# Performance work log

Measured on AMD Instinct MI355X. Metric: run time of the kernel, lower is better.

Reference implementation:

```python
import jax, jax.numpy as jnp
import numpy as np

N = 100000        # nodes
E = 1600000       # edges
DIM = 64
HEADS = 8
HEAD_DIM = DIM // HEADS
HIDDEN = 4 * DIM  # hidden_dim_multiplier = 4


def setup_inputs() -> dict:
    key = jax.random.key(0)
    ks = jax.random.split(key, 20)
    s = 0.05
    return {
        "x": jax.random.normal(ks[0], (N, DIM), jnp.float32),
        "edge_feat": jax.random.normal(ks[1], (E, 2), jnp.float32),
        "w_in": jax.random.normal(ks[2], (DIM, DIM), jnp.float32) * s,
        "b_in": jnp.zeros((DIM,), jnp.float32),
        "w_edge": jax.random.normal(ks[3], (2, DIM), jnp.float32) * s,
        "b_edge": jnp.zeros((DIM,), jnp.float32),
        "w_att_u": jax.random.normal(ks[4], (DIM, HEADS), jnp.float32) * s,
        "b_att_u": jnp.zeros((HEADS,), jnp.float32),
        "w_att_v": jax.random.normal(ks[5], (DIM, HEADS), jnp.float32) * s,  # no bias
        "w_att_e": jax.random.normal(ks[6], (DIM, HEADS), jnp.float32) * s,
        "b_att_e": jnp.zeros((HEADS,), jnp.float32),
        "w_ff1": jax.random.normal(ks[7], (DIM, HIDDEN), jnp.float32) * s,
        "b_ff1": jnp.zeros((HIDDEN,), jnp.float32),
        "w_ff2": jax.random.normal(ks[8], (HIDDEN, DIM), jnp.float32) * s,
        "b_ff2": jnp.zeros((DIM,), jnp.float32),
        "src": jax.random.randint(ks[9], (E,), 0, N, jnp.int32),
        "dst": jax.random.randint(ks[10], (E,), 0, N, jnp.int32),
    }


def reference(x, edge_feat, w_in, b_in, w_edge, b_edge, w_att_u, b_att_u,
              w_att_v, w_att_e, b_att_e, w_ff1, b_ff1, w_ff2, b_ff2, src, dst):
    n = x.shape[0]
    h = x @ w_in + b_in                                  # [N, dim]
    ea = edge_feat @ w_edge + b_edge                     # [E, dim]
    su = h @ w_att_u + b_att_u                           # [N, H]
    sv = h @ w_att_v                                     # [N, H] (no bias)
    se = ea @ w_att_e + b_att_e                          # [E, H]
    # u_add_v gather + edge bias + LeakyReLU
    scores = jax.nn.leaky_relu(su[src] + sv[dst] + se, 0.2)  # [E, H]
    # edge softmax over incoming edges of each dst node
    m = jax.ops.segment_max(scores, dst, num_segments=n)     # [N, H]
    m = jnp.where(jnp.isfinite(m), m, 0.0)                   # nodes w/o in-edges
    e = jnp.exp(scores - m[dst])                             # [E, H]
    denom = jax.ops.segment_sum(e, dst, num_segments=n)      # [N, H]
    probs = e / jnp.maximum(denom, 1e-12)[dst]               # [E, H]
    # u_mul_e_sum: weighted scatter-sum of messages
    hv = h.reshape(n, HEAD_DIM, HEADS)                       # [N, hd, H]
    msg = hv[src] * probs[:, None, :]                        # [E, hd, H]
    out = jax.ops.segment_sum(msg, dst, num_segments=n).reshape(n, DIM)
    # feed-forward (dropout=0 at eval)
    out = jax.nn.gelu(out @ w_ff1 + b_ff1, approximate=False) @ w_ff2 + b_ff2
    return out
```

## Files before the change

### kernel.cpp

```cpp
#include <hip/hip_runtime.h>
#include <math.h>

#define DIM 64
#define HEADS 8
#define HIDDEN 256

__device__ __forceinline__ float lane_bcast(float v, int srcLane) {
  return __int_as_float(__builtin_amdgcn_readlane(__float_as_int(v), srcLane));
}

__global__ void prep_kernel(
    const float* __restrict__ w_in, const float* __restrict__ b_in,
    const float* __restrict__ w_edge, const float* __restrict__ b_edge,
    const float* __restrict__ w_att_u, const float* __restrict__ b_att_u,
    const float* __restrict__ w_att_v,
    const float* __restrict__ w_att_e, const float* __restrict__ b_att_e,
    float* __restrict__ Waug, float* __restrict__ baug,
    float* __restrict__ wcc, float* __restrict__ bcc)
{
  int t = threadIdx.x;
  if (t < 64) {
    for (int j = 0; j < 64; ++j) Waug[t*80 + j] = w_in[t*64 + j];
    for (int hh = 0; hh < 8; ++hh) {
      float a = 0.f, b = 0.f;
      for (int j = 0; j < 64; ++j) {
        float w = w_in[t*64 + j];
        a += w * w_att_u[j*8 + hh];
        b += w * w_att_v[j*8 + hh];
      }
      Waug[t*80 + 64 + hh] = a;
      Waug[t*80 + 72 + hh] = b;
    }
  } else if (t < 128) {
    int j = t - 64;
    baug[j] = b_in[j];
  } else if (t < 136) {
    int hh = t - 128;
    float a = b_att_u[hh];
    for (int k = 0; k < 64; ++k) a += b_in[k] * w_att_u[k*8 + hh];
    baug[64 + hh] = a;
  } else if (t < 144) {
    int hh = t - 136;
    float a = 0.f;
    for (int k = 0; k < 64; ++k) a += b_in[k] * w_att_v[k*8 + hh];
    baug[72 + hh] = a;
  } else if (t < 160) {
    int c = (t - 144) >> 3, hh = (t - 144) & 7;
    float a = 0.f;
    for (int j = 0; j < 64; ++j) a += w_edge[c*64 + j] * w_att_e[j*8 + hh];
    wcc[c*8 + hh] = a;
  } else if (t < 168) {
    int hh = t - 160;
    float a = b_att_e[hh];
    for (int j = 0; j < 64; ++j) a += b_edge[j] * w_att_e[j*8 + hh];
    bcc[hh] = a;
  }
}

__global__ __launch_bounds__(256) void node_gemm_kernel(
    const float* __restrict__ x,
    const float* __restrict__ Waug, const float* __restrict__ baug,
    float* __restrict__ hbuf, float* __restrict__ subuf, float* __restrict__ svbuf,
    int n_nodes)
{
  const int wid = threadIdx.x >> 6;
  const int lane = threadIdx.x & 63;
  const long nbase = (long)blockIdx.x * 32 + wid * 8;

  float xr[8];
  #pragma unroll
  for (int m = 0; m < 8; ++m) {
    long n = nbase + m; if (n >= n_nodes) n = n_nodes - 1;
    xr[m] = x[n*DIM + lane];
  }
  const float bmain = baug[lane];
  const float bext  = (lane < 16) ? baug[64 + lane] : 0.f;
  float acc[8], acc2[8];
  #pragma unroll
  for (int m = 0; m < 8; ++m) { acc[m] = bmain; acc2[m] = 0.f; }

  #pragma unroll 16
  for (int k = 0; k < 64; ++k) {
    float wmain = Waug[k*80 + lane];
    float wext  = (lane < 16) ? Waug[k*80 + 64 + lane] : 0.f;
    #pragma unroll
    for (int m = 0; m < 8; ++m) {
      float xk = lane_bcast(xr[m], k);
      acc[m]  += xk * wmain;
      acc2[m] += xk * wext;
    }
  }
  #pragma unroll
  for (int m = 0; m < 8; ++m) {
    long n = nbase + m;
    if (n >= n_nodes) continue;
    hbuf[n*DIM + lane] = acc[m];
    if (lane < 8)       subuf[n*8 + lane]     = acc2[m] + bext;
    else if (lane < 16) svbuf[n*8 + lane - 8] = acc2[m] + bext;
  }
}

__global__ void hist_kernel(const int* __restrict__ dst, int* __restrict__ deg, int n_edges) {
  int i = blockIdx.x * blockDim.x + threadIdx.x;
  if (i < n_edges) atomicAdd(&deg[dst[i]], 1);
}

__global__ void alloc_kernel(const int* __restrict__ deg, int* __restrict__ off,
                             int* __restrict__ counter, int n_nodes) {
  int i = blockIdx.x * blockDim.x + threadIdx.x;
  int lane = threadIdx.x & 63;
  int d = (i < n_nodes) ? deg[i] : 0;
  int pre = d;
  #pragma unroll
  for (int s = 1; s < 64; s <<= 1) {
    int v = __shfl_up(pre, s, 64);
    if (lane >= s) pre += v;
  }
  int tot = __shfl(pre, 63, 64);
  int base = 0;
  if (lane == 0) base = atomicAdd(counter, tot);
  base = __shfl(base, 0, 64);
  if (i < n_nodes) off[i] = base + pre - d;
}

__global__ void scatter_kernel(const int* __restrict__ dst, const int* __restrict__ off,
                               int* __restrict__ pos, int* __restrict__ csr, int n_edges) {
  int i = blockIdx.x * blockDim.x + threadIdx.x;
  if (i < n_edges) {
    int d = dst[i];
    int p = atomicAdd(&pos[d], 1);
    csr[off[d] + p] = i;
  }
}

__global__ __launch_bounds__(256) void attn_kernel(
    const int* __restrict__ src, const int* __restrict__ csr,
    const int* __restrict__ off, const int* __restrict__ deg,
    const float* __restrict__ edge_feat,
    const float* __restrict__ hbuf, const float* __restrict__ subuf,
    const float* __restrict__ svbuf,
    const float* __restrict__ wcc, const float* __restrict__ bcc,
    float* __restrict__ agg, int n_nodes)
{
  __shared__ float pbuf[4][4][16][8];
  __shared__ int   sbuf[4][4][16];
  const int wid = threadIdx.x >> 6;
  const int lane = threadIdx.x & 63;
  const int g = lane >> 4, sub = lane & 15;
  const long n = (long)blockIdx.x * 16 + wid * 4 + g;
  const bool valid = (n < n_nodes);
  const long nc = valid ? n : (long)(n_nodes - 1);
  const int ebase = off[nc];
  const int d = valid ? deg[nc] : 0;
  const int hb = (sub & 1) * 4;

  float svn[8], c0v[8], c1v[8], cbv[8];
  {
    const float4* svp = (const float4*)(svbuf + nc*8);
    float4 s0 = svp[0], s1 = svp[1];
    svn[0]=s0.x; svn[1]=s0.y; svn[2]=s0.z; svn[3]=s0.w;
    svn[4]=s1.x; svn[5]=s1.y; svn[6]=s1.z; svn[7]=s1.w;
    #pragma unroll
    for (int hh = 0; hh < 8; ++hh) {
      c0v[hh] = wcc[hh]; c1v[hh] = wcc[8+hh]; cbv[hh] = bcc[hh];
    }
  }
  float m8[8], den8[8];
  #pragma unroll
  for (int hh = 0; hh < 8; ++hh) { m8[hh] = -INFINITY; den8[hh] = 0.f; }
  float4 msg = make_float4(0.f, 0.f, 0.f, 0.f);

  for (int c0 = 0; c0 < d; c0 += 16) {
    const int cnt = min(16, d - c0);
    float sc[8];
    int sid = 0;
    if (sub < cnt) {
      const int eid = csr[ebase + c0 + sub];
      sid = src[eid];
      const float2 ef = *(const float2*)(edge_feat + (long)eid*2);
      const float4* sup = (const float4*)(subuf + (long)sid*8);
      float4 u0 = sup[0], u1 = sup[1];
      float suv[8] = {u0.x,u0.y,u0.z,u0.w,u1.x,u1.y,u1.z,u1.w};
      #pragma unroll
      for (int hh = 0; hh < 8; ++hh) {
        float v = suv[hh] + svn[hh] + ef.x*c0v[hh] + ef.y*c1v[hh] + cbv[hh];
        sc[hh] = (v > 0.f) ? v : 0.2f*v;
      }
    } else {
      #pragma unroll
      for (int hh = 0; hh < 8; ++hh) sc[hh] = -INFINITY;
    }
    float cm[8];
    #pragma unroll
    for (int hh = 0; hh < 8; ++hh) cm[hh] = sc[hh];
    #pragma unroll
    for (int sft = 8; sft >= 1; sft >>= 1) {
      #pragma unroll
      for (int hh = 0; hh < 8; ++hh)
        cm[hh] = fmaxf(cm[hh], __shfl_xor(cm[hh], sft, 64));
    }
    float f[8], pv[8];
    #pragma unroll
    for (int hh = 0; hh < 8; ++hh) {
      float nm = fmaxf(m8[hh], cm[hh]);
      f[hh] = __expf(m8[hh] - nm);
      pv[hh] = __expf(sc[hh] - nm);
      m8[hh] = nm;
    }
    if (sub < cnt) {
      float4* pp = (float4*)&pbuf[wid][g][sub][0];
      pp[0] = make_float4(pv[0], pv[1], pv[2], pv[3]);
      pp[1] = make_float4(pv[4], pv[5], pv[6], pv[7]);
      sbuf[wid][g][sub] = sid;
    }
    float q[8];
    #pragma unroll
    for (int hh = 0; hh < 8; ++hh) q[hh] = pv[hh];
    #pragma unroll
    for (int sft = 8; sft >= 1; sft >>= 1) {
      #pragma unroll
      for (int hh = 0; hh < 8; ++hh)
        q[hh] += __shfl_xor(q[hh], sft, 64);
    }
    #pragma unroll
    for (int hh = 0; hh < 8; ++hh) den8[hh] = den8[hh]*f[hh] + q[hh];
    {
      float f0 = (sub & 1) ? f[4] : f[0];
      float f1 = (sub & 1) ? f[5] : f[1];
      float f2 = (sub & 1) ? f[6] : f[2];
      float f3 = (sub & 1) ? f[7] : f[3];
      msg.x *= f0; msg.y *= f1; msg.z *= f2; msg.w *= f3;
    }
    asm volatile("s_waitcnt lgkmcnt(0)" ::: "memory");

    #pragma unroll 2
    for (int e2 = 0; e2 < cnt; ++e2) {
      int sidu = sbuf[wid][g][e2];
      float4 p = *(const float4*)&pbuf[wid][g][e2][hb];
      float4 hv = *(const float4*)&hbuf[(long)sidu*DIM + sub*4];
      msg.x += hv.x*p.x; msg.y += hv.y*p.y; msg.z += hv.z*p.z; msg.w += hv.w*p.w;
    }
  }
  float d0 = (sub & 1) ? den8[4] : den8[0];
  float d1 = (sub & 1) ? den8[5] : den8[1];
  float d2 = (sub & 1) ? den8[6] : den8[2];
  float d3 = (sub & 1) ? den8[7] : den8[3];
  if (valid) {
    float4 o;
    o.x = msg.x / fmaxf(d0, 1e-12f);
    o.y = msg.y / fmaxf(d1, 1e-12f);
    o.z = msg.z / fmaxf(d2, 1e-12f);
    o.w = msg.w / fmaxf(d3, 1e-12f);
    *(float4*)(agg + n*DIM + sub*4) = o;
  }
}

__global__ __launch_bounds__(256) void ffn1_kernel(
    const float* __restrict__ agg,
    const float* __restrict__ w1, const float* __restrict__ b1,
    float* __restrict__ g, int n_nodes)
{
  const int wid  = __builtin_amdgcn_readfirstlane(threadIdx.x >> 6);
  const int lane = threadIdx.x & 63;
  const long nbase = (long)blockIdx.x * 32 + wid * 8;

  const float* xrow[8];
  #pragma unroll
  for (int m = 0; m < 8; ++m) {
    long n = nbase + m; if (n >= n_nodes) n = n_nodes - 1;
    xrow[m] = agg + n*DIM;
  }
  float4 bb = *(const float4*)(b1 + lane*4);
  float h[8][4];
  #pragma unroll
  for (int m = 0; m < 8; ++m) { h[m][0]=bb.x; h[m][1]=bb.y; h[m][2]=bb.z; h[m][3]=bb.w; }

  #pragma unroll 8
  for (int k = 0; k < 64; ++k) {
    float4 w = *(const float4*)(w1 + k*HIDDEN + lane*4);
    #pragma unroll
    for (int m = 0; m < 8; ++m) {
      float xk = xrow[m][k];
      h[m][0] += xk*w.x; h[m][1] += xk*w.y; h[m][2] += xk*w.z; h[m][3] += xk*w.w;
    }
  }
  #pragma unroll
  for (int m = 0; m < 8; ++m) {
    long n = nbase + m;
    if (n >= n_nodes) continue;
    float4 o;
    o.x = 0.5f*h[m][0]*(1.0f + erff(h[m][0]*0.70710678118654752f));
    o.y = 0.5f*h[m][1]*(1.0f + erff(h[m][1]*0.70710678118654752f));
    o.z = 0.5f*h[m][2]*(1.0f + erff(h[m][2]*0.70710678118654752f));
    o.w = 0.5f*h[m][3]*(1.0f + erff(h[m][3]*0.70710678118654752f));
    *(float4*)(g + n*HIDDEN + lane*4) = o;
  }
}

__global__ __launch_bounds__(256) void ffn2_kernel(
    const float* __restrict__ g,
    const float* __restrict__ w2, const float* __restrict__ b2,
    float* __restrict__ out, int n_nodes)
{
  const int wid  = __builtin_amdgcn_readfirstlane(threadIdx.x >> 6);
  const int lane = threadIdx.x & 63;
  const long nbase = (long)blockIdx.x * 32 + wid * 8;

  const float* grow[8];
  #pragma unroll
  for (int m = 0; m < 8; ++m) {
    long n = nbase + m; if (n >= n_nodes) n = n_nodes - 1;
    grow[m] = g + n*HIDDEN;
  }
  const float b2v = b2[lane];
  float acc[8];
  #pragma unroll
  for (int m = 0; m < 8; ++m) acc[m] = b2v;

  #pragma unroll 8
  for (int j = 0; j < HIDDEN; ++j) {
    float wv = w2[j*DIM + lane];
    #pragma unroll
    for (int m = 0; m < 8; ++m)
      acc[m] += grow[m][j] * wv;
  }
  #pragma unroll
  for (int m = 0; m < 8; ++m) {
    long n = nbase + m;
    if (n < n_nodes) out[n*DIM + lane] = acc[m];
  }
}

extern "C" void kernel_launch(void* const* d_in, const int* in_sizes, int n_in,
                              void* d_out, int out_size, void* d_ws, size_t ws_size,
                              hipStream_t stream)
{
  const float* x         = (const float*)d_in[0];
  const float* edge_feat = (const float*)d_in[1];
  const float* w_in      = (const float*)d_in[2];
  const float* b_in      = (const float*)d_in[3];
  const float* w_edge    = (const float*)d_in[4];
  const float* b_edge    = (const float*)d_in[5];
  const float* w_att_u   = (const float*)d_in[6];
  const float* b_att_u   = (const float*)d_in[7];
  const float* w_att_v   = (const float*)d_in[8];
  const float* w_att_e   = (const float*)d_in[9];
  const float* b_att_e   = (const float*)d_in[10];
  const float* w_ff1     = (const float*)d_in[11];
  const float* b_ff1     = (const float*)d_in[12];
  const float* w_ff2     = (const float*)d_in[13];
  const float* b_ff2     = (const float*)d_in[14];
  const int*   src       = (const int*)d_in[15];
  const int*   dst       = (const int*)d_in[16];
  float* out = (float*)d_out;

  const int n_nodes = in_sizes[0] / DIM;
  const int n_edges = in_sizes[15];

  char* p = (char*)d_ws;
  auto alloc_f = [&](size_t cnt) { float* r = (float*)p; p += ((cnt*4 + 255) & ~(size_t)255); return r; };
  auto alloc_i = [&](size_t cnt) { int* r = (int*)p;   p += ((cnt*4 + 255) & ~(size_t)255); return r; };
  float* Waug  = alloc_f(64*80);
  float* baug  = alloc_f(80);
  float* wcc   = alloc_f(16);
  float* bcc   = alloc_f(8);
  float* aggb  = alloc_f((size_t)n_nodes*DIM);
  float* hbuf  = alloc_f((size_t)n_nodes*DIM);
  float* subuf = alloc_f((size_t)n_nodes*8);
  float* svbuf = alloc_f((size_t)n_nodes*8);
  int* deg     = alloc_i(n_nodes);
  int* pos     = alloc_i(n_nodes);
  int* counter = alloc_i(64);
  int* offb    = alloc_i(n_nodes);
  int* csr     = alloc_i(n_edges);
  float* gbuf  = hbuf;

  hipMemsetAsync(deg, 0, (size_t)((char*)offb - (char*)deg), stream);

  hipLaunchKernelGGL(prep_kernel, dim3(1), dim3(256), 0, stream,
      w_in, b_in, w_edge, b_edge, w_att_u, b_att_u, w_att_v, w_att_e, b_att_e,
      Waug, baug, wcc, bcc);

  hipLaunchKernelGGL(node_gemm_kernel, dim3((n_nodes+31)/32), dim3(256), 0, stream,
      x, Waug, baug, hbuf, subuf, svbuf, n_nodes);

  hipLaunchKernelGGL(hist_kernel, dim3((n_edges+255)/256), dim3(256), 0, stream,
      dst, deg, n_edges);
  hipLaunchKernelGGL(alloc_kernel, dim3((n_nodes+255)/256), dim3(256), 0, stream,
      deg, offb, counter, n_nodes);
  hipLaunchKernelGGL(scatter_kernel, dim3((n_edges+255)/256), dim3(256), 0, stream,
      dst, offb, pos, csr, n_edges);

  hipLaunchKernelGGL(attn_kernel, dim3((n_nodes+15)/16), dim3(256), 0, stream,
      src, csr, offb, deg, edge_feat, hbuf, subuf, svbuf, wcc, bcc, aggb, n_nodes);

  hipLaunchKernelGGL(ffn1_kernel, dim3((n_nodes+31)/32), dim3(256), 0, stream,
      aggb, w_ff1, b_ff1, gbuf, n_nodes);

  hipLaunchKernelGGL(ffn2_kernel, dim3((n_nodes+31)/32), dim3(256), 0, stream,
      gbuf, w_ff2, b_ff2, out, n_nodes);
}
```

Baseline: 632.2 us.

## Store gather tables in fp16, pack edge records, swizzle LDS, enlarge FFN tiles

The node projection and source attention scores are now stored in half precision, which halves the bytes gathered per edge in the attention kernel. The scatter step builds packed 16-byte edge records holding src and the edge features, so the attention kernel no longer makes the indirect csr->src->edge_feat loads. The shared-memory layout for probabilities is transposed and XOR-swizzled to reduce bank conflicts. The FFN kernels now handle 16 rows per wave instead of 8, with adjusted unrolling. In exchange, fp16 storage reduces accuracy, the larger FFN tiles raise register pressure, and the record array adds scatter-side write traffic.

```diff
diff --git a/kernel.cpp b/kernel.cpp
--- a/kernel.cpp
+++ b/kernel.cpp
@@ -1,9 +1,13 @@
 #include <hip/hip_runtime.h>
+#include <hip/hip_fp16.h>
 #include <math.h>
 
 #define DIM 64
 #define HEADS 8
 #define HIDDEN 256
+
+struct h2x2 { __half2 a, b; };
+struct h2x4 { __half2 a, b, c, d; };
 
 __device__ __forceinline__ float lane_bcast(float v, int srcLane) {
   return __int_as_float(__builtin_amdgcn_readlane(__float_as_int(v), srcLane));
@@ -60,8 +64,8 @@
 __global__ __launch_bounds__(256) void node_gemm_kernel(
     const float* __restrict__ x,
     const float* __restrict__ Waug, const float* __restrict__ baug,
-    float* __restrict__ hbuf, float* __restrict__ subuf, float* __restrict__ svbuf,
-    int n_nodes)
+    __half* __restrict__ hbuf16, __half* __restrict__ subuf16,
+    float* __restrict__ svbuf, int n_nodes)
 {
   const int wid = threadIdx.x >> 6;
   const int lane = threadIdx.x & 63;
@@ -94,8 +98,8 @@
   for (int m = 0; m < 8; ++m) {
     long n = nbase + m;
     if (n >= n_nodes) continue;
-    hbuf[n*DIM + lane] = acc[m];
-    if (lane < 8)       subuf[n*8 + lane]     = acc2[m] + bext;
+    hbuf16[n*DIM + lane] = __float2half(acc[m]);
+    if (lane < 8)       subuf16[n*8 + lane]   = __float2half(acc2[m] + bext);
     else if (lane < 16) svbuf[n*8 + lane - 8] = acc2[m] + bext;
   }
 }
@@ -123,27 +127,34 @@
   if (i < n_nodes) off[i] = base + pre - d;
 }
 
-__global__ void scatter_kernel(const int* __restrict__ dst, const int* __restrict__ off,
-                               int* __restrict__ pos, int* __restrict__ csr, int n_edges) {
+__global__ void scatter_kernel(const int* __restrict__ dst, const int* __restrict__ src,
+                               const float* __restrict__ edge_feat,
+                               const int* __restrict__ off,
+                               int* __restrict__ pos, int4* __restrict__ recs, int n_edges) {
   int i = blockIdx.x * blockDim.x + threadIdx.x;
   if (i < n_edges) {
     int d = dst[i];
     int p = atomicAdd(&pos[d], 1);
-    csr[off[d] + p] = i;
+    float2 ef = *(const float2*)(edge_feat + (long)i*2);
+    int4 rec;
+    rec.x = src[i];
+    rec.y = __float_as_int(ef.x);
+    rec.z = __float_as_int(ef.y);
+    rec.w = 0;
+    recs[off[d] + p] = rec;
   }
 }
 
 __global__ __launch_bounds__(256) void attn_kernel(
-    const int* __restrict__ src, const int* __restrict__ csr,
+    const int4* __restrict__ recs,
     const int* __restrict__ off, const int* __restrict__ deg,
-    const float* __restrict__ edge_feat,
-    const float* __restrict__ hbuf, const float* __restrict__ subuf,
+    const __half* __restrict__ hbuf16, const __half* __restrict__ subuf16,
     const float* __restrict__ svbuf,
     const float* __restrict__ wcc, const float* __restrict__ bcc,
     float* __restrict__ agg, int n_nodes)
 {
-  __shared__ float pbuf[4][4][16][8];
-  __shared__ int   sbuf[4][4][16];
+  __shared__ float pbuf[4][16][4][8];
+  __shared__ int   sbuf[4][16][4];
   const int wid = threadIdx.x >> 6;
   const int lane = threadIdx.x & 63;
   const int g = lane >> 4, sub = lane & 15;
@@ -175,15 +186,16 @@
     float sc[8];
     int sid = 0;
     if (sub < cnt) {
-      const int eid = csr[ebase + c0 + sub];
-      sid = src[eid];
-      const float2 ef = *(const float2*)(edge_feat + (long)eid*2);
-      const float4* sup = (const float4*)(subuf + (long)sid*8);
-      float4 u0 = sup[0], u1 = sup[1];
-      float suv[8] = {u0.x,u0.y,u0.z,u0.w,u1.x,u1.y,u1.z,u1.w};
+      int4 rec = recs[ebase + c0 + sub];
+      sid = rec.x;
+      float efx = __int_as_float(rec.y), efy = __int_as_float(rec.z);
+      h2x4 up = *(const h2x4*)(subuf16 + (long)sid*8);
+      float2 u0 = __half22float2(up.a), u1 = __half22float2(up.b);
+      float2 u2 = __half22float2(up.c), u3 = __half22float2(up.d);
+      float suv[8] = {u0.x,u0.y,u1.x,u1.y,u2.x,u2.y,u3.x,u3.y};
       #pragma unroll
       for (int hh = 0; hh < 8; ++hh) {
-        float v = suv[hh] + svn[hh] + ef.x*c0v[hh] + ef.y*c1v[hh] + cbv[hh];
+        float v = suv[hh] + svn[hh] + efx*c0v[hh] + efy*c1v[hh] + cbv[hh];
         sc[hh] = (v > 0.f) ? v : 0.2f*v;
       }
     } else {
@@ -208,10 +220,10 @@
       m8[hh] = nm;
     }
     if (sub < cnt) {
-      float4* pp = (float4*)&pbuf[wid][g][sub][0];
+      float4* pp = (float4*)&pbuf[wid][sub][g ^ (sub & 3)][0];
       pp[0] = make_float4(pv[0], pv[1], pv[2], pv[3]);
       pp[1] = make_float4(pv[4], pv[5], pv[6], pv[7]);
-      sbuf[wid][g][sub] = sid;
+      sbuf[wid][sub][g ^ (sub & 3)] = sid;
     }
     float q[8];
     #pragma unroll
@@ -233,12 +245,14 @@
     }
     asm volatile("s_waitcnt lgkmcnt(0)" ::: "memory");
 
-    #pragma unroll 2
+    #pragma unroll 4
     for (int e2 = 0; e2 < cnt; ++e2) {
-      int sidu = sbuf[wid][g][e2];
-      float4 p = *(const float4*)&pbuf[wid][g][e2][hb];
-      float4 hv = *(const float4*)&hbuf[(long)sidu*DIM + sub*4];
-      msg.x += hv.x*p.x; msg.y += hv.y*p.y; msg.z += hv.z*p.z; msg.w += hv.w*p.w;
+      const int gs = g ^ (e2 & 3);
+      int sidu = sbuf[wid][e2][gs];
+      float4 p = *(const float4*)&pbuf[wid][e2][gs][hb];
+      h2x2 hv = *(const h2x2*)(hbuf16 + (long)sidu*DIM + sub*4);
+      float2 h01 = __half22float2(hv.a), h23 = __half22float2(hv.b);
+      msg.x += h01.x*p.x; msg.y += h01.y*p.y; msg.z += h23.x*p.z; msg.w += h23.y*p.w;
     }
   }
   float d0 = (sub & 1) ? den8[4] : den8[0];
@@ -262,30 +276,30 @@
 {
   const int wid  = __builtin_amdgcn_readfirstlane(threadIdx.x >> 6);
   const int lane = threadIdx.x & 63;
-  const long nbase = (long)blockIdx.x * 32 + wid * 8;
-
-  const float* xrow[8];
-  #pragma unroll
-  for (int m = 0; m < 8; ++m) {
+  const long nbase = (long)blockIdx.x * 64 + wid * 16;
+
+  const float* xrow[16];
+  #pragma unroll
+  for (int m = 0; m < 16; ++m) {
     long n = nbase + m; if (n >= n_nodes) n = n_nodes - 1;
     xrow[m] = agg + n*DIM;
   }
   float4 bb = *(const float4*)(b1 + lane*4);
-  float h[8][4];
-  #pragma unroll
-  for (int m = 0; m < 8; ++m) { h[m][0]=bb.x; h[m][1]=bb.y; h[m][2]=bb.z; h[m][3]=bb.w; }
-
-  #pragma unroll 8
+  float h[16][4];
+  #pragma unroll
+  for (int m = 0; m < 16; ++m) { h[m][0]=bb.x; h[m][1]=bb.y; h[m][2]=bb.z; h[m][3]=bb.w; }
+
+  #pragma unroll 4
   for (int k = 0; k < 64; ++k) {
     float4 w = *(const float4*)(w1 + k*HIDDEN + lane*4);
     #pragma unroll
-    for (int m = 0; m < 8; ++m) {
+    for (int m = 0; m < 16; ++m) {
       float xk = xrow[m][k];
       h[m][0] += xk*w.x; h[m][1] += xk*w.y; h[m][2] += xk*w.z; h[m][3] += xk*w.w;
     }
   }
   #pragma unroll
-  for (int m = 0; m < 8; ++m) {
+  for (int m = 0; m < 16; ++m) {
     long n = nbase + m;
     if (n >= n_nodes) continue;
     float4 o;
@@ -304,28 +318,28 @@
 {
   const int wid  = __builtin_amdgcn_readfirstlane(threadIdx.x >> 6);
   const int lane = threadIdx.x & 63;
-  const long nbase = (long)blockIdx.x * 32 + wid * 8;
-
-  const float* grow[8];
-  #pragma unroll
-  for (int m = 0; m < 8; ++m) {
+  const long nbase = (long)blockIdx.x * 64 + wid * 16;
+
+  const float* grow[16];
+  #pragma unroll
+  for (int m = 0; m < 16; ++m) {
     long n = nbase + m; if (n >= n_nodes) n = n_nodes - 1;
     grow[m] = g + n*HIDDEN;
   }
   const float b2v = b2[lane];
-  float acc[8];
-  #pragma unroll
-  for (int m = 0; m < 8; ++m) acc[m] = b2v;
-
-  #pragma unroll 8
+  float acc[16];
+  #pragma unroll
+  for (int m = 0; m < 16; ++m) acc[m] = b2v;
+
+  #pragma unroll 4
   for (int j = 0; j < HIDDEN; ++j) {
     float wv = w2[j*DIM + lane];
     #pragma unroll
-    for (int m = 0; m < 8; ++m)
+    for (int m = 0; m < 16; ++m)
       acc[m] += grow[m][j] * wv;
   }
   #pragma unroll
-  for (int m = 0; m < 8; ++m) {
+  for (int m = 0; m < 16; ++m) {
     long n = nbase + m;
     if (n < n_nodes) out[n*DIM + lane] = acc[m];
   }
@@ -358,22 +372,21 @@
   const int n_edges = in_sizes[15];
 
   char* p = (char*)d_ws;
-  auto alloc_f = [&](size_t cnt) { float* r = (float*)p; p += ((cnt*4 + 255) & ~(size_t)255); return r; };
-  auto alloc_i = [&](size_t cnt) { int* r = (int*)p;   p += ((cnt*4 + 255) & ~(size_t)255); return r; };
-  float* Waug  = alloc_f(64*80);
-  float* baug  = alloc_f(80);
-  float* wcc   = alloc_f(16);
-  float* bcc   = alloc_f(8);
-  float* aggb  = alloc_f((size_t)n_nodes*DIM);
-  float* hbuf  = alloc_f((size_t)n_nodes*DIM);
-  float* subuf = alloc_f((size_t)n_nodes*8);
-  float* svbuf = alloc_f((size_t)n_nodes*8);
-  int* deg     = alloc_i(n_nodes);
-  int* pos     = alloc_i(n_nodes);
-  int* counter = alloc_i(64);
-  int* offb    = alloc_i(n_nodes);
-  int* csr     = alloc_i(n_edges);
-  float* gbuf  = hbuf;
+  auto alloc_b = [&](size_t bytes) { char* r = p; p += ((bytes + 255) & ~(size_t)255); return r; };
+  float*  Waug    = (float*)alloc_b(64*80*4);
+  float*  baug    = (float*)alloc_b(80*4);
+  float*  wcc     = (float*)alloc_b(16*4);
+  float*  bcc     = (float*)alloc_b(8*4);
+  float*  aggb    = (float*)alloc_b((size_t)n_nodes*DIM*4);
+  __half* hbuf16  = (__half*)alloc_b((size_t)n_nodes*DIM*2);
+  __half* subuf16 = (__half*)alloc_b((size_t)n_nodes*8*2);
+  float*  svbuf   = (float*)alloc_b((size_t)n_nodes*8*4);
+  int*    deg     = (int*)alloc_b((size_t)n_nodes*4);
+  int*    pos     = (int*)alloc_b((size_t)n_nodes*4);
+  int*    counter = (int*)alloc_b(256);
+  int*    offb    = (int*)alloc_b((size_t)n_nodes*4);
+  int4*   recs    = (int4*)alloc_b((size_t)n_edges*16);
+  float*  gbuf    = (float*)hbuf16;
 
   hipMemsetAsync(deg, 0, (size_t)((char*)offb - (char*)deg), stream);
 
@@ -382,21 +395,21 @@
       Waug, baug, wcc, bcc);
 
   hipLaunchKernelGGL(node_gemm_kernel, dim3((n_nodes+31)/32), dim3(256), 0, stream,
-      x, Waug, baug, hbuf, subuf, svbuf, n_nodes);
+      x, Waug, baug, hbuf16, subuf16, svbuf, n_nodes);
 
   hipLaunchKernelGGL(hist_kernel, dim3((n_edges+255)/256), dim3(256), 0, stream,
       dst, deg, n_edges);
   hipLaunchKernelGGL(alloc_kernel, dim3((n_nodes+255)/256), dim3(256), 0, stream,
       deg, offb, counter, n_nodes);
   hipLaunchKernelGGL(scatter_kernel, dim3((n_edges+255)/256), dim3(256), 0, stream,
-      dst, offb, pos, csr, n_edges);
+      dst, src, edge_feat, offb, pos, recs, n_edges);
 
   hipLaunchKernelGGL(attn_kernel, dim3((n_nodes+15)/16), dim3(256), 0, stream,
-      src, csr, offb, deg, edge_feat, hbuf, subuf, svbuf, wcc, bcc, aggb, n_nodes);
-
-  hipLaunchKernelGGL(ffn1_kernel, dim3((n_nodes+31)/32), dim3(256), 0, stream,
+      recs, offb, deg, hbuf16, subuf16, svbuf, wcc, bcc, aggb, n_nodes);
+
+  hipLaunchKernelGGL(ffn1_kernel, dim3((n_nodes+63)/64), dim3(256), 0, stream,
       aggb, w_ff1, b_ff1, gbuf, n_nodes);
 
-  hipLaunchKernelGGL(ffn2_kernel, dim3((n_nodes+31)/32), dim3(256), 0, stream,
+  hipLaunchKernelGGL(ffn2_kernel, dim3((n_nodes+63)/64), dim3(256), 0, stream,
       gbuf, w_ff2, b_ff2, out, n_nodes);
 }
```

After: 654.8 us. 1.04x slower.
